# Kernel tuning notes

Hardware: AMD Instinct MI355X
Metric: run time of the kernel (lower is better)

The kernel has to match this reference:

```python
import jax, jax.numpy as jnp
import numpy as np

B = 8192
DB, DA, DE, DM, DS = 512, 256, 256, 512, 512
IN = DB + DA + DE + DM + DS  # 2048
F = 2048


def _ternary_linear(x, w, b):
    # BitNet-b1.58 absmean quantization with straight-through estimator.
    s = jnp.mean(jnp.abs(w))
    wq = jnp.round(jnp.clip(w / (s + 1e-5), -1.0, 1.0)) * s
    wq = w + jax.lax.stop_gradient(wq - w)  # STE
    return x @ wq.T + b


def _layernorm(x, g, b, eps=1e-5):
    m = jnp.mean(x, axis=-1, keepdims=True)
    v = jnp.mean((x - m) ** 2, axis=-1, keepdims=True)
    return (x - m) * jax.lax.rsqrt(v + eps) * g + b


def _gelu(x):
    return jax.nn.gelu(x, approximate=False)  # torch nn.GELU default (erf)


def setup_inputs() -> dict:
    key = jax.random.key(0)
    ks = jax.random.split(key, 16)
    w = lambda k, o, i: (jax.random.normal(k, (o, i), dtype=jnp.float32) * 0.02)
    return {
        "z_byte": jax.random.normal(ks[0], (B, DB), dtype=jnp.float32),
        "z_addr": jax.random.normal(ks[1], (B, DA), dtype=jnp.float32),
        "z_evt": jax.random.normal(ks[2], (B, DE), dtype=jnp.float32),
        "z_map": jax.random.normal(ks[3], (B, DM), dtype=jnp.float32),
        "z_sum": jax.random.normal(ks[4], (B, DS), dtype=jnp.float32),
        "gate_w1": w(ks[5], F, IN), "gate_b1": jnp.zeros((F,), jnp.float32),
        "gate_w2": w(ks[6], F, F), "gate_b2": jnp.zeros((F,), jnp.float32),
        "tr_w1": w(ks[7], F, IN), "tr_b1": jnp.zeros((F,), jnp.float32),
        "tr_w2": w(ks[8], F, F), "tr_b2": jnp.zeros((F,), jnp.float32),
        "mlp_w1": w(ks[9], 2 * F, F), "mlp_b1": jnp.zeros((2 * F,), jnp.float32),
        "mlp_w2": w(ks[10], F, 2 * F), "mlp_b2": jnp.zeros((F,), jnp.float32),
        "ln1_g": jnp.ones((F,), jnp.float32), "ln1_b": jnp.zeros((F,), jnp.float32),
        "ln2_g": jnp.ones((F,), jnp.float32), "ln2_b": jnp.zeros((F,), jnp.float32),
    }


def reference(z_byte, z_addr, z_evt, z_map, z_sum,
              gate_w1, gate_b1, gate_w2, gate_b2,
              tr_w1, tr_b1, tr_w2, tr_b2,
              mlp_w1, mlp_b1, mlp_w2, mlp_b2,
              ln1_g, ln1_b, ln2_g, ln2_b):
    combined = jnp.concatenate([z_byte, z_addr, z_evt, z_map, z_sum], axis=-1)  # [B, IN]
    g = _ternary_linear(_gelu(_ternary_linear(combined, gate_w1, gate_b1)), gate_w2, gate_b2)
    t = _ternary_linear(_gelu(_ternary_linear(combined, tr_w1, tr_b1)), tr_w2, tr_b2)
    fused = jax.nn.sigmoid(g * 1.2) * t
    fused = _layernorm(fused, ln1_g, ln1_b)
    mlp = _gelu(fused @ mlp_w1.T + mlp_b1) @ mlp_w2.T + mlp_b2
    return _layernorm(fused + mlp, ln2_g, ln2_b)
```

## Files before the change

### kernel.cpp

```cpp
#include <hip/hip_runtime.h>

typedef unsigned short u16;
typedef unsigned int u32;
typedef __bf16 bf16x8 __attribute__((ext_vector_type(8)));
typedef float f32x4 __attribute__((ext_vector_type(4)));

#define B_ROWS 8192

__device__ __forceinline__ float bf2f(u16 h) {
    union { u32 u; float f; } v; v.u = ((u32)h) << 16; return v.f;
}
__device__ __forceinline__ u16 f2bf(float f) {
    union { float f; u32 u; } v; v.f = f;
    u32 r = v.u + 0x7fffu + ((v.u >> 16) & 1u);
    return (u16)(r >> 16);
}
__device__ __forceinline__ float gelu_fast(float x) {
    float u = x * (0.7978845608f + 0.0356774081f * x * x);
    float e = __expf(2.f * u);
    float th = 1.f - 2.f / (e + 1.f);
    return 0.5f * x * (1.f + th);
}
__device__ __forceinline__ float sigmoid12(float g) {
    return 1.f / (1.f + __expf(-1.2f * g));
}
__device__ __forceinline__ float wave_reduce_sum(float v) {
    #pragma unroll
    for (int m = 32; m; m >>= 1) v += __shfl_xor(v, m, 64);
    return v;
}
__device__ __forceinline__ void async16(const void* g, void* l) {
    __builtin_amdgcn_global_load_lds((const __attribute__((address_space(1))) u32*)g,
                                     (__attribute__((address_space(3))) u32*)l, 16, 0, 0);
}

__global__ void absmean1_kernel(const float* __restrict__ w0, const float* __restrict__ w1,
                                const float* __restrict__ w2, const float* __restrict__ w3,
                                float* __restrict__ partials) {
    const float* w = (blockIdx.y == 0) ? w0 : (blockIdx.y == 1) ? w1 : (blockIdx.y == 2) ? w2 : w3;
    int base = blockIdx.x * 16384;
    float acc = 0.f;
    for (int j = threadIdx.x; j < 16384; j += 256) {
        float4 v = ((const float4*)w)[base + j];
        acc += fabsf(v.x) + fabsf(v.y) + fabsf(v.z) + fabsf(v.w);
    }
    acc = wave_reduce_sum(acc);
    __shared__ float red[4];
    int lane = threadIdx.x & 63, wv = threadIdx.x >> 6;
    if (lane == 0) red[wv] = acc;
    __syncthreads();
    if (threadIdx.x == 0)
        partials[blockIdx.y * 64 + blockIdx.x] = red[0] + red[1] + red[2] + red[3];
}

__global__ void absmean2_kernel(const float* __restrict__ partials, double* __restrict__ sums) {
    float v = partials[blockIdx.x * 64 + threadIdx.x];
    v = wave_reduce_sum(v);
    if (threadIdx.x == 0) sums[blockIdx.x] = (double)v;
}

__global__ void prep_kernel(const float* __restrict__ w0, const float* __restrict__ w1,
                            const float* __restrict__ w2, const float* __restrict__ w3,
                            const float* __restrict__ mw1, const float* __restrict__ mw2,
                            u16* __restrict__ wq, u16* __restrict__ mwq,
                            const double* __restrict__ sums) {
    int y = blockIdx.y;
    int i = blockIdx.x * 256 + threadIdx.x;
    if (y < 4) {
        const float* w = (y == 0) ? w0 : (y == 1) ? w1 : (y == 2) ? w2 : w3;
        float s = (float)(sums[y] * (1.0 / 4194304.0));
        float den = s + 1e-5f;
        float4 v = ((const float4*)w)[i];
        ushort4 o;
        o.x = f2bf(rintf(fminf(fmaxf(v.x / den, -1.f), 1.f)));
        o.y = f2bf(rintf(fminf(fmaxf(v.y / den, -1.f), 1.f)));
        o.z = f2bf(rintf(fminf(fmaxf(v.z / den, -1.f), 1.f)));
        o.w = f2bf(rintf(fminf(fmaxf(v.w / den, -1.f), 1.f)));
        ((ushort4*)(wq + (size_t)y * 4194304))[i] = o;
    } else {
        const float* src = (y == 4) ? mw1 : mw2;
        u16* dst = mwq + (y == 4 ? 0 : 8388608);
        #pragma unroll
        for (int r = 0; r < 2; ++r) {
            int j = i + r * 1048576;
            float4 v = ((const float4*)src)[j];
            ushort4 o = {f2bf(v.x), f2bf(v.y), f2bf(v.z), f2bf(v.w)};
            ((ushort4*)dst)[j] = o;
        }
    }
}

__global__ void concat_kernel(const float* __restrict__ zb, const float* __restrict__ za,
                              const float* __restrict__ ze, const float* __restrict__ zm,
                              const float* __restrict__ zs, u16* __restrict__ out) {
    int row = blockIdx.x, t = threadIdx.x;
    int col = t * 8;
    const float* src; int scol, stride;
    if (col < 512)       { src = zb; scol = col;        stride = 512; }
    else if (col < 768)  { src = za; scol = col - 512;  stride = 256; }
    else if (col < 1024) { src = ze; scol = col - 768;  stride = 256; }
    else if (col < 1536) { src = zm; scol = col - 1024; stride = 512; }
    else                 { src = zs; scol = col - 1536; stride = 512; }
    const float4* s4 = (const float4*)(src + (size_t)row * stride + scol);
    float4 a = s4[0], b = s4[1];
    ushort4 p0 = {f2bf(a.x), f2bf(a.y), f2bf(a.z), f2bf(a.w)};
    ushort4 p1 = {f2bf(b.x), f2bf(b.y), f2bf(b.z), f2bf(b.w)};
    u16* o = out + (size_t)row * 2048 + col;
    *(ushort4*)o = p0;
    *(ushort4*)(o + 4) = p1;
}

#define STG_A(d, h, kt_) { \
    async16(Ab0 + (size_t)(h) * ha + (size_t)(kt_) * 64, &lds[d][0][h][ci0 * 8]); \
    async16(Ab1 + (size_t)(h) * ha + (size_t)(kt_) * 64, &lds[d][0][h][ci1 * 8]); }
#define STG_B(d, h, kt_) { \
    async16(Wb0 + (size_t)(h) * hw + (size_t)(kt_) * 64, &lds[d][1][h][ci0 * 8]); \
    async16(Wb1 + (size_t)(h) * hw + (size_t)(kt_) * 64, &lds[d][1][h][ci1 * 8]); }
#define LDA_ALL(d, qm) { \
    const u16* p_ = &lds[d][0][qm][r0a * 64]; \
    af[0][0] = *(const bf16x8*)(p_ + cA0);        af[0][1] = *(const bf16x8*)(p_ + cA1); \
    af[1][0] = *(const bf16x8*)(p_ + 1024 + cA0); af[1][1] = *(const bf16x8*)(p_ + 1024 + cA1); \
    af[2][0] = *(const bf16x8*)(p_ + 2048 + cA0); af[2][1] = *(const bf16x8*)(p_ + 2048 + cA1); \
    af[3][0] = *(const bf16x8*)(p_ + 3072 + cA0); af[3][1] = *(const bf16x8*)(p_ + 3072 + cA1); }
#define LDB_H(d, qn) { \
    const u16* p_ = &lds[d][1][qn][r0b * 64]; \
    bf[qn][0][0] = *(const bf16x8*)(p_ + cB0);        bf[qn][0][1] = *(const bf16x8*)(p_ + cB1); \
    bf[qn][1][0] = *(const bf16x8*)(p_ + 1024 + cB0); bf[qn][1][1] = *(const bf16x8*)(p_ + 1024 + cB1); }
#define MFMA_PH(qm, qn) { \
    _Pragma("unroll") for (int fm = 0; fm < 4; ++fm) \
    _Pragma("unroll") for (int fn = 0; fn < 2; ++fn) { \
        acc[qm][qn][fm][fn] = __builtin_amdgcn_mfma_f32_16x16x32_bf16(af[fm][0], bf[qn][fn][0], acc[qm][qn][fm][fn], 0, 0, 0); \
        acc[qm][qn][fm][fn] = __builtin_amdgcn_mfma_f32_16x16x32_bf16(af[fm][1], bf[qn][fn][1], acc[qm][qn][fm][fn], 0, 0, 0); } }
#define PH_TAIL(qm, qn) \
    __builtin_amdgcn_s_barrier(); \
    asm volatile("s_waitcnt lgkmcnt(0)" ::: "memory"); \
    __builtin_amdgcn_sched_barrier(0); \
    __builtin_amdgcn_s_setprio(1); \
    MFMA_PH(qm, qn); \
    __builtin_amdgcn_s_setprio(0); \
    __builtin_amdgcn_s_barrier();
#define GROUP(ktv, d, e) { \
    LDA_ALL(d, 0); LDB_H(d, 0); \
    if ((ktv) + 1 < NT) { STG_B(e, 0, (ktv) + 1); STG_A(e, 1, (ktv) + 1); } \
    PH_TAIL(0, 0); \
    LDB_H(d, 1); \
    PH_TAIL(0, 1); \
    LDA_ALL(d, 1); \
    if ((ktv) + 2 < NT) STG_A(d, 0, (ktv) + 2); \
    PH_TAIL(1, 1); \
    if ((ktv) + 2 < NT) STG_B(d, 1, (ktv) + 2); \
    __builtin_amdgcn_s_barrier(); \
    __builtin_amdgcn_s_setprio(1); \
    MFMA_PH(1, 0); \
    __builtin_amdgcn_s_setprio(0); \
    if ((ktv) < NT - 2)       { asm volatile("s_waitcnt vmcnt(4)" ::: "memory"); } \
    else if ((ktv) == NT - 2) { asm volatile("s_waitcnt vmcnt(0)" ::: "memory"); } \
    __builtin_amdgcn_s_barrier(); }

template<int EPI>
__global__ __launch_bounds__(512, 2) void gemm256(
        const u16* __restrict__ A, const u16* __restrict__ A2, int lda,
        const u16* __restrict__ W, int wz,
        const float* __restrict__ bias0, const float* __restrict__ bias1,
        void* out, void* out2,
        const double* sum0, const double* sum1,
        int N, int K, int ncut) {
    __shared__ __align__(16) u16 lds[2][2][2][8192];
    if (blockIdx.z) { A = A2; W += wz; out = out2; bias0 = bias1; sum0 = sum1; }

    const int t = threadIdx.x;
    const int l = t & 63;
    const int w = t >> 6;
    const int lr = l & 15, quad = l >> 4;
    const int wm = w >> 2, wn = w & 3;
    const int bn0 = blockIdx.x * 256, bm0 = blockIdx.y * 256;
    const int NT = K >> 6;

    const int ci0 = t, ci1 = 512 + t;
    const int row0 = ci0 >> 3, row1 = ci1 >> 3;
    const int cg0 = (ci0 & 7) ^ (row0 & 7);
    const int cg1 = (ci1 & 7) ^ (row1 & 7);
    const u16* Ab0 = A + (size_t)(bm0 + row0) * lda + cg0 * 8;
    const u16* Ab1 = A + (size_t)(bm0 + row1) * lda + cg1 * 8;
    const u16* Wb0 = W + (size_t)(bn0 + row0) * K + cg0 * 8;
    const u16* Wb1 = W + (size_t)(bn0 + row1) * K + cg1 * 8;
    const size_t ha = (size_t)128 * lda;
    const size_t hw = (size_t)128 * K;

    const int r0a = wm * 64 + lr;
    const int xa = r0a & 7;
    const int cA0 = ((quad) ^ xa) * 8, cA1 = ((4 + quad) ^ xa) * 8;
    const int r0b = wn * 32 + lr;
    const int xb = r0b & 7;
    const int cB0 = ((quad) ^ xb) * 8, cB1 = ((4 + quad) ^ xb) * 8;

    f32x4 acc[2][2][4][2] = {};
    bf16x8 af[4][2];
    bf16x8 bf[2][2][2];

    STG_A(0, 0, 0); STG_B(0, 0, 0); STG_B(0, 1, 0); STG_A(0, 1, 0);
    asm volatile("" ::: "memory");
    STG_A(1, 0, 1); STG_B(1, 1, 1);
    asm volatile("s_waitcnt vmcnt(4)" ::: "memory");
    __builtin_amdgcn_s_barrier();

    for (int kt = 0; kt < NT; kt += 2) {
        GROUP(kt, 0, 1);
        GROUP(kt + 1, 1, 0);
    }

    float s0 = sum0 ? (float)(*sum0 * (1.0 / 4194304.0)) : 1.f;
    float s1 = sum1 ? (float)(*sum1 * (1.0 / 4194304.0)) : 1.f;
    #pragma unroll
    for (int qn = 0; qn < 2; ++qn) {
        #pragma unroll
        for (int fn = 0; fn < 2; ++fn) {
            int gcol = bn0 + qn * 128 + wn * 32 + fn * 16 + lr;
            bool lo = gcol < ncut;
            float bv = lo ? bias0[gcol] : bias1[gcol - ncut];
            float sc = lo ? s0 : s1;
            #pragma unroll
            for (int qm = 0; qm < 2; ++qm) {
                #pragma unroll
                for (int fm = 0; fm < 4; ++fm) {
                    #pragma unroll
                    for (int i = 0; i < 4; ++i) {
                        int grow = bm0 + qm * 128 + wm * 64 + fm * 16 + quad * 4 + i;
                        size_t idx = (size_t)grow * N + gcol;
                        float v = acc[qm][qn][fm][fn][i] * sc + bv;
                        if (EPI == 0)      ((u16*)out)[idx]   = f2bf(gelu_fast(v));
                        else if (EPI == 1) ((float*)out)[idx] = v;
                        else               ((u16*)out)[idx]   = f2bf(v);
                    }
                }
            }
        }
    }
}

__global__ void ln1_kernel(const u16* __restrict__ g, const u16* tt,
                           u16* outb,
                           const float* __restrict__ gam, const float* __restrict__ bet) {
    int row = blockIdx.x, t = threadIdx.x;
    int c0 = t * 8;
    uint4 gv = *(const uint4*)(g  + (size_t)row * 2048 + c0);
    uint4 tv = *(const uint4*)(tt + (size_t)row * 2048 + c0);
    u32 gw[4] = {gv.x, gv.y, gv.z, gv.w}, tw[4] = {tv.x, tv.y, tv.z, tv.w};
    float f[8];
    #pragma unroll
    for (int j = 0; j < 4; ++j) {
        f[2 * j]     = sigmoid12(bf2f((u16)(gw[j] & 0xffff))) * bf2f((u16)(tw[j] & 0xffff));
        f[2 * j + 1] = sigmoid12(bf2f((u16)(gw[j] >> 16)))    * bf2f((u16)(tw[j] >> 16));
    }
    float s1 = 0.f, s2 = 0.f;
    #pragma unroll
    for (int j = 0; j < 8; ++j) { s1 += f[j]; s2 += f[j] * f[j]; }
    s1 = wave_reduce_sum(s1); s2 = wave_reduce_sum(s2);
    __shared__ float red[8];
    int lane = t & 63, wv = t >> 6;
    if (lane == 0) { red[wv] = s1; red[4 + wv] = s2; }
    __syncthreads();
    float S1 = red[0] + red[1] + red[2] + red[3];
    float S2 = red[4] + red[5] + red[6] + red[7];
    float mean = S1 * (1.f / 2048.f);
    float var = S2 * (1.f / 2048.f) - mean * mean;
    float r = rsqrtf(var + 1e-5f);
    u16 ob[8];
    #pragma unroll
    for (int j = 0; j < 8; ++j)
        ob[j] = f2bf((f[j] - mean) * r * gam[c0 + j] + bet[c0 + j]);
    *(uint4*)(outb + (size_t)row * 2048 + c0) = *(uint4*)ob;
}

__global__ void ln2_kernel(const u16* __restrict__ fb, float* io,
                           const float* __restrict__ gam, const float* __restrict__ bet) {
    int row = blockIdx.x, t = threadIdx.x;
    int c0 = t * 8;
    uint4 fv = *(const uint4*)(fb + (size_t)row * 2048 + c0);
    u32 fw[4] = {fv.x, fv.y, fv.z, fv.w};
    float4* iov = (float4*)(io + (size_t)row * 2048 + c0);
    float4 m0 = iov[0], m1 = iov[1];
    float x[8] = {m0.x, m0.y, m0.z, m0.w, m1.x, m1.y, m1.z, m1.w};
    #pragma unroll
    for (int j = 0; j < 4; ++j) {
        x[2 * j]     += bf2f((u16)(fw[j] & 0xffff));
        x[2 * j + 1] += bf2f((u16)(fw[j] >> 16));
    }
    float s1 = 0.f, s2 = 0.f;
    #pragma unroll
    for (int j = 0; j < 8; ++j) { s1 += x[j]; s2 += x[j] * x[j]; }
    s1 = wave_reduce_sum(s1); s2 = wave_reduce_sum(s2);
    __shared__ float red[8];
    int lane = t & 63, wv = t >> 6;
    if (lane == 0) { red[wv] = s1; red[4 + wv] = s2; }
    __syncthreads();
    float S1 = red[0] + red[1] + red[2] + red[3];
    float S2 = red[4] + red[5] + red[6] + red[7];
    float mean = S1 * (1.f / 2048.f);
    float var = S2 * (1.f / 2048.f) - mean * mean;
    float r = rsqrtf(var + 1e-5f);
    float o[8];
    #pragma unroll
    for (int j = 0; j < 8; ++j)
        o[j] = (x[j] - mean) * r * gam[c0 + j] + bet[c0 + j];
    iov[0] = make_float4(o[0], o[1], o[2], o[3]);
    iov[1] = make_float4(o[4], o[5], o[6], o[7]);
}

extern "C" void kernel_launch(void* const* d_in, const int* in_sizes, int n_in,
                              void* d_out, int out_size, void* d_ws, size_t ws_size,
                              hipStream_t stream) {
    const float* zb  = (const float*)d_in[0];
    const float* za  = (const float*)d_in[1];
    const float* ze  = (const float*)d_in[2];
    const float* zm  = (const float*)d_in[3];
    const float* zs  = (const float*)d_in[4];
    const float* gw1 = (const float*)d_in[5];  const float* gb1 = (const float*)d_in[6];
    const float* gw2 = (const float*)d_in[7];  const float* gb2 = (const float*)d_in[8];
    const float* tw1 = (const float*)d_in[9];  const float* tb1 = (const float*)d_in[10];
    const float* tw2 = (const float*)d_in[11]; const float* tb2 = (const float*)d_in[12];
    const float* mw1 = (const float*)d_in[13]; const float* mb1 = (const float*)d_in[14];
    const float* mw2 = (const float*)d_in[15]; const float* mb2 = (const float*)d_in[16];
    const float* l1g = (const float*)d_in[17]; const float* l1b = (const float*)d_in[18];
    const float* l2g = (const float*)d_in[19]; const float* l2b = (const float*)d_in[20];

    char* wsb = (char*)d_ws;
    u16*   combined = (u16*)(wsb + 0);
    u16*   gbuf     = (u16*)(wsb + 0);
    u16*   wq       = (u16*)(wsb + 33554432);
    u16*   tbuf     = (u16*)(wsb + 67108864);
    u16*   fusedb   = (u16*)(wsb + 67108864);
    u16*   mwq      = (u16*)(wsb + 100663296);
    u16*   HgHt     = (u16*)(wsb + 134217728);
    u16*   M1       = (u16*)(wsb + 134217728);
    float* partials = (float*)(wsb + 134217728);
    double* sums    = (double*)(wsb + 201326592);
    float* mlp2     = (float*)d_out;

    absmean1_kernel<<<dim3(64, 4), 256, 0, stream>>>(gw1, tw1, gw2, tw2, partials);
    absmean2_kernel<<<4, 64, 0, stream>>>(partials, sums);
    prep_kernel<<<dim3(4096, 6), 256, 0, stream>>>(gw1, tw1, gw2, tw2, mw1, mw2, wq, mwq, sums);
    concat_kernel<<<B_ROWS, 256, 0, stream>>>(zb, za, ze, zm, zs, combined);

    gemm256<0><<<dim3(16, 32, 1), 512, 0, stream>>>(
        combined, nullptr, 2048, wq, 0, gb1, tb1, HgHt, nullptr,
        &sums[0], &sums[1], 4096, 2048, 2048);
    gemm256<3><<<dim3(8, 32, 2), 512, 0, stream>>>(
        HgHt, HgHt + 2048, 4096, wq + 8388608, 4194304, gb2, tb2, gbuf, tbuf,
        &sums[2], &sums[3], 2048, 2048, 2048);
    ln1_kernel<<<B_ROWS, 256, 0, stream>>>(gbuf, tbuf, fusedb, l1g, l1b);
    gemm256<0><<<dim3(16, 32, 1), 512, 0, stream>>>(
        fusedb, nullptr, 2048, mwq, 0, mb1, mb1, M1, nullptr,
        nullptr, nullptr, 4096, 2048, 4096);
    gemm256<1><<<dim3(8, 32, 1), 512, 0, stream>>>(
        M1, nullptr, 4096, mwq + 8388608, 0, mb2, mb2, mlp2, nullptr,
        nullptr, nullptr, 2048, 4096, 2048);
    ln2_kernel<<<B_ROWS, 256, 0, stream>>>(fusedb, mlp2, l2g, l2b);
}
```

Before: 833.5 us.

## Use immediate-offset LDS reads and swizzle workgroup tile order

Reorders the LDS buffer so all A and B fragment reads come from four base pointers with compile-time immediate offsets in inline ds_read_b128, which removes per-read address arithmetic and frees VGPRs. It also remaps the flat workgroup id so that consecutive workgroups are spread in strides across the grid, with the aim of improving L2 reuse of A and W tiles. The inline asm with memory clobbers may limit how the compiler schedules the reads, and the swizzle assumes the grid size is divisible by 8.

```diff
diff --git a/kernel.cpp b/kernel.cpp
--- a/kernel.cpp
+++ b/kernel.cpp
@@ -4,6 +4,7 @@
 typedef unsigned int u32;
 typedef __bf16 bf16x8 __attribute__((ext_vector_type(8)));
 typedef float f32x4 __attribute__((ext_vector_type(4)));
+typedef const __attribute__((address_space(3))) u16* ldsp;
 
 #define B_ROWS 8192
 
@@ -32,6 +33,13 @@
 __device__ __forceinline__ void async16(const void* g, void* l) {
     __builtin_amdgcn_global_load_lds((const __attribute__((address_space(1))) u32*)g,
                                      (__attribute__((address_space(3))) u32*)l, 16, 0, 0);
+}
+template<int OFF>
+__device__ __forceinline__ bf16x8 dsr(ldsp a) {
+    bf16x8 r;
+    asm volatile("ds_read_b128 %0, %1 offset:%c2"
+                 : "=v"(r) : "v"(a), "i"(OFF) : "memory");
+    return r;
 }
 
 __global__ void absmean1_kernel(const float* __restrict__ w0, const float* __restrict__ w1,
@@ -111,21 +119,21 @@
 }
 
 #define STG_A(d, h, kt_) { \
-    async16(Ab0 + (size_t)(h) * ha + (size_t)(kt_) * 64, &lds[d][0][h][ci0 * 8]); \
-    async16(Ab1 + (size_t)(h) * ha + (size_t)(kt_) * 64, &lds[d][0][h][ci1 * 8]); }
+    async16(Ab0 + (size_t)(h) * ha + (size_t)(kt_) * 64, &lds[0][d][h][ci0 * 8]); \
+    async16(Ab1 + (size_t)(h) * ha + (size_t)(kt_) * 64, &lds[0][d][h][ci1 * 8]); }
 #define STG_B(d, h, kt_) { \
-    async16(Wb0 + (size_t)(h) * hw + (size_t)(kt_) * 64, &lds[d][1][h][ci0 * 8]); \
-    async16(Wb1 + (size_t)(h) * hw + (size_t)(kt_) * 64, &lds[d][1][h][ci1 * 8]); }
+    async16(Wb0 + (size_t)(h) * hw + (size_t)(kt_) * 64, &lds[1][d][h][ci0 * 8]); \
+    async16(Wb1 + (size_t)(h) * hw + (size_t)(kt_) * 64, &lds[1][d][h][ci1 * 8]); }
+#define AOFF(d, qm, fm) (((d) * 2 + (qm)) * 16384 + (fm) * 2048)
+#define BOFF(d, qn, fn) (((d) * 2 + (qn)) * 16384 + (fn) * 2048)
 #define LDA_ALL(d, qm) { \
-    const u16* p_ = &lds[d][0][qm][r0a * 64]; \
-    af[0][0] = *(const bf16x8*)(p_ + cA0);        af[0][1] = *(const bf16x8*)(p_ + cA1); \
-    af[1][0] = *(const bf16x8*)(p_ + 1024 + cA0); af[1][1] = *(const bf16x8*)(p_ + 1024 + cA1); \
-    af[2][0] = *(const bf16x8*)(p_ + 2048 + cA0); af[2][1] = *(const bf16x8*)(p_ + 2048 + cA1); \
-    af[3][0] = *(const bf16x8*)(p_ + 3072 + cA0); af[3][1] = *(const bf16x8*)(p_ + 3072 + cA1); }
+    af[0][0] = dsr<AOFF(d,qm,0)>(vA0); af[0][1] = dsr<AOFF(d,qm,0)>(vA1); \
+    af[1][0] = dsr<AOFF(d,qm,1)>(vA0); af[1][1] = dsr<AOFF(d,qm,1)>(vA1); \
+    af[2][0] = dsr<AOFF(d,qm,2)>(vA0); af[2][1] = dsr<AOFF(d,qm,2)>(vA1); \
+    af[3][0] = dsr<AOFF(d,qm,3)>(vA0); af[3][1] = dsr<AOFF(d,qm,3)>(vA1); }
 #define LDB_H(d, qn) { \
-    const u16* p_ = &lds[d][1][qn][r0b * 64]; \
-    bf[qn][0][0] = *(const bf16x8*)(p_ + cB0);        bf[qn][0][1] = *(const bf16x8*)(p_ + cB1); \
-    bf[qn][1][0] = *(const bf16x8*)(p_ + 1024 + cB0); bf[qn][1][1] = *(const bf16x8*)(p_ + 1024 + cB1); }
+    bf[qn][0][0] = dsr<BOFF(d,qn,0)>(vB0); bf[qn][0][1] = dsr<BOFF(d,qn,0)>(vB1); \
+    bf[qn][1][0] = dsr<BOFF(d,qn,1)>(vB0); bf[qn][1][1] = dsr<BOFF(d,qn,1)>(vB1); }
 #define MFMA_PH(qm, qn) { \
     _Pragma("unroll") for (int fm = 0; fm < 4; ++fm) \
     _Pragma("unroll") for (int fn = 0; fn < 2; ++fn) { \
@@ -173,8 +181,12 @@
     const int w = t >> 6;
     const int lr = l & 15, quad = l >> 4;
     const int wm = w >> 2, wn = w & 3;
-    const int bn0 = blockIdx.x * 256, bm0 = blockIdx.y * 256;
     const int NT = K >> 6;
+
+    const int nwg  = gridDim.x * gridDim.y;
+    const int flat = blockIdx.y * gridDim.x + blockIdx.x;
+    const int swz  = (flat & 7) * (nwg >> 3) + (flat >> 3);
+    const int bn0 = (swz % gridDim.x) * 256, bm0 = (swz / gridDim.x) * 256;
 
     const int ci0 = t, ci1 = 512 + t;
     const int row0 = ci0 >> 3, row1 = ci1 >> 3;
@@ -188,11 +200,14 @@
     const size_t hw = (size_t)128 * K;
 
     const int r0a = wm * 64 + lr;
-    const int xa = r0a & 7;
-    const int cA0 = ((quad) ^ xa) * 8, cA1 = ((4 + quad) ^ xa) * 8;
+    const int cA0u = ((quad) ^ (r0a & 7)) * 8;
     const int r0b = wn * 32 + lr;
-    const int xb = r0b & 7;
-    const int cB0 = ((quad) ^ xb) * 8, cB1 = ((4 + quad) ^ xb) * 8;
+    const int cB0u = ((quad) ^ (r0b & 7)) * 8;
+    ldsp lb = (ldsp)&lds[0][0][0][0];
+    ldsp vA0 = lb + r0a * 64 + cA0u;
+    ldsp vA1 = lb + r0a * 64 + (cA0u ^ 32);
+    ldsp vB0 = lb + 32768 + r0b * 64 + cB0u;
+    ldsp vB1 = lb + 32768 + r0b * 64 + (cB0u ^ 32);
 
     f32x4 acc[2][2][4][2] = {};
     bf16x8 af[4][2];
```

Measured after the change: 818.9 us. Within noise of the previous version (-1.8%).
